# Kernel tuning notes

Hardware: AMD Instinct MI355X
Metric: run time of the kernel (lower is better)

Reference implementation:

```python
import jax, jax.numpy as jnp
import numpy as np

N_NODES = 100000


def gcn_conv(x, src, dst, W, b, n):
    """PyG GCNConv: add self-loops, symmetric normalization, out = A_hat @ (x W) + b."""
    loop = jnp.arange(n, dtype=src.dtype)
    s = jnp.concatenate([src, loop])
    d = jnp.concatenate([dst, loop])
    deg = jnp.zeros((n,), dtype=x.dtype).at[d].add(1.0)
    dinv = jnp.where(deg > 0, jax.lax.rsqrt(deg), 0.0)
    norm = dinv[s] * dinv[d]                      # [E+N]
    h = x @ W                                     # [N, out]
    msg = h[s] * norm[:, None]                    # [E+N, out] gather
    out = jax.ops.segment_sum(msg, d, num_segments=n)  # scatter-add
    return out + b


def prelu(x, a):
    return jnp.where(x >= 0, x, a * x)


def setup_inputs() -> dict:
    key = jax.random.key(0)
    ks = jax.random.split(key, 12)
    n, din, dout, dproj = N_NODES, 128, 128, 128
    dhid = 2 * dout
    x = jax.random.normal(ks[0], (n, din), dtype=jnp.float32)
    edge_index = jax.random.randint(ks[1], (2, 1600000), 0, n, dtype=jnp.int64)

    def glorot(k, fan_in, fan_out):
        lim = np.sqrt(6.0 / (fan_in + fan_out))
        return jax.random.uniform(k, (fan_in, fan_out), jnp.float32, -lim, lim)

    return {
        "x": x,
        "edge_index": edge_index,
        "W1": glorot(ks[2], din, dhid),
        "b1": jnp.zeros((dhid,), jnp.float32),
        "W2": glorot(ks[3], dhid, dout),
        "b2": jnp.zeros((dout,), jnp.float32),
        "a": jnp.asarray(0.25, jnp.float32),          # PReLU weight (num_parameters=1)
        "fc1_w": glorot(ks[4], dout, dproj),
        "fc1_b": jnp.zeros((dproj,), jnp.float32),
        "fc2_w": glorot(ks[5], dproj, dout),
        "fc2_b": jnp.zeros((dout,), jnp.float32),
    }


def reference(x, edge_index, W1, b1, W2, b2, a, fc1_w, fc1_b, fc2_w, fc2_b):
    n = x.shape[0]
    src, dst = edge_index[0], edge_index[1]
    out = prelu(gcn_conv(x, src, dst, W1, b1, n), a)
    out = prelu(gcn_conv(out, src, dst, W2, b2, n), a)
    proj = jax.nn.relu(out @ fc1_w + fc1_b)
    proj = proj @ fc2_w + fc2_b
    return (out, proj)
```

## Files before the change

### kernel.cpp

```cpp
#include <hip/hip_runtime.h>


typedef __attribute__((ext_vector_type(4))) float  f32x4;
typedef __attribute__((ext_vector_type(8))) __bf16 bf16x8;
typedef __attribute__((ext_vector_type(8))) short  short8;

__device__ __forceinline__ bf16x8 as_bf(short8 s) {
    union { short8 s; bf16x8 b; } u; u.s = s; return u.b;
}

__device__ __forceinline__ short2 split1(float x) {
    unsigned u = __float_as_uint(x);
    short hi = (short)(u >> 16);
    float hif = __uint_as_float(u & 0xFFFF0000u);
    short lo = (short)(__float_as_uint(x - hif) >> 16);
    return make_short2(hi, lo);
}

__global__ void deg_kernel(const int* __restrict__ dst, int* __restrict__ deg, int E) {
    int e = blockIdx.x * blockDim.x + threadIdx.x;
    if (e < E) atomicAdd(&deg[dst[e]], 1);
}

__global__ __launch_bounds__(256)
void part_kernel(const int* __restrict__ deg, int* __restrict__ bsum,
                 float* __restrict__ dinv, int n) {
    int tid = threadIdx.x;
    int base = blockIdx.x * 1024 + tid * 4;
    int d[4] = {0, 0, 0, 0};
    if (base + 3 < n) {
        int4 v = *(const int4*)(deg + base);
        d[0] = v.x; d[1] = v.y; d[2] = v.z; d[3] = v.w;
    } else {
        for (int j = 0; j < 4; ++j) if (base + j < n) d[j] = deg[base + j];
    }
    for (int j = 0; j < 4; ++j)
        if (base + j < n) dinv[base + j] = rsqrtf((float)(d[j] + 1));
    int s = d[0] + d[1] + d[2] + d[3];
    for (int off = 32; off > 0; off >>= 1) s += __shfl_down(s, off);
    __shared__ int wsum[4];
    if ((tid & 63) == 0) wsum[tid >> 6] = s;
    __syncthreads();
    if (tid == 0) bsum[blockIdx.x] = wsum[0] + wsum[1] + wsum[2] + wsum[3];
}

__global__ __launch_bounds__(1024)
void topscan_kernel(const int* __restrict__ bsum, int* __restrict__ bbase, int nb) {
    __shared__ int sh[1024];
    int tid = threadIdx.x;
    int own = (tid < nb) ? bsum[tid] : 0;
    sh[tid] = own;
    __syncthreads();
    for (int off = 1; off < 1024; off <<= 1) {
        int t = (tid >= off) ? sh[tid - off] : 0;
        __syncthreads();
        sh[tid] += t;
        __syncthreads();
    }
    if (tid < nb) bbase[tid] = sh[tid] - own;
}

__global__ __launch_bounds__(256)
void offs_kernel(const int* __restrict__ deg, const int* __restrict__ bbase,
                 int* __restrict__ offsets, int n) {
    int tid = threadIdx.x;
    int base = blockIdx.x * 1024 + tid * 4;
    int d[4] = {0, 0, 0, 0};
    if (base + 3 < n) {
        int4 v = *(const int4*)(deg + base);
        d[0] = v.x; d[1] = v.y; d[2] = v.z; d[3] = v.w;
    } else {
        for (int j = 0; j < 4; ++j) if (base + j < n) d[j] = deg[base + j];
    }
    int s = d[0] + d[1] + d[2] + d[3];
    __shared__ int sh[256];
    sh[tid] = s;
    __syncthreads();
    for (int off = 1; off < 256; off <<= 1) {
        int t = (tid >= off) ? sh[tid - off] : 0;
        __syncthreads();
        sh[tid] += t;
        __syncthreads();
    }
    int run = bbase[blockIdx.x] + sh[tid] - s;
    for (int j = 0; j < 4; ++j) {
        int idx = base + j;
        if (idx <= n) offsets[idx] = run;
        if (idx < n) run += d[j];
    }
}

__global__ void fill_kernel(const int* __restrict__ src, const int* __restrict__ dst,
                            const int* __restrict__ offsets, int* __restrict__ cursor,
                            int* __restrict__ csr, int E) {
    int e = blockIdx.x * blockDim.x + threadIdx.x;
    if (e < E) {
        int d = dst[e];
        int pos = offsets[d] + atomicAdd(&cursor[d], 1);
        csr[pos] = src[e];
    }
}

__global__ void wconv_kernel(const float* __restrict__ W, short* __restrict__ Fh,
                             short* __restrict__ Fl, int K, int N, int ktlog) {
    int o = blockIdx.x * blockDim.x + threadIdx.x;
    if (o >= K * N) return;
    int j  = o & 7;
    int l  = (o >> 3) & 15;
    int q  = (o >> 7) & 3;
    int t2 = o >> 9;
    int kt = t2 & ((1 << ktlog) - 1);
    int nt = t2 >> ktlog;
    int nn = nt * 16 + l;
    int kk = kt * 32 + q * 8 + j;
    short2 s = split1(W[(size_t)kk * N + nn]);
    Fh[o] = s.x;
    Fl[o] = s.y;
}

__global__ __launch_bounds__(256)
void agg128_kernel(const float* __restrict__ g, const int* __restrict__ csr,
                   const int* __restrict__ offsets, const float* __restrict__ dinv,
                   const float* __restrict__ bias, const float* __restrict__ a_ptr,
                   float* __restrict__ out, int n) {
    int w = threadIdx.x >> 6;
    int lane = threadIdx.x & 63;
    int v = blockIdx.x * 4 + w;
    if (v >= n) return;
    const char* gb = (const char*)g;
    unsigned loff = (unsigned)lane * 8u;
    float dv = dinv[v];
    float2 self = *(const float2*)(gb + ((unsigned)v * 512u + loff));
    float accx = dv * self.x;
    float accy = dv * self.y;
    int e = offsets[v], end = offsets[v + 1];
#pragma unroll 1
    for (; e < end; e += 12) {
        int   idx[12];
        float dd[12];
        float2 mm[12];
#pragma unroll
        for (int j = 0; j < 12; ++j) {
            int ee = e + j;
            idx[j] = csr[ee < end ? ee : end - 1];
        }
#pragma unroll
        for (int j = 0; j < 12; ++j)
            dd[j] = (e + j < end) ? dinv[idx[j]] : 0.f;
#pragma unroll
        for (int j = 0; j < 12; ++j)
            mm[j] = *(const float2*)(gb + ((unsigned)idx[j] * 512u + loff));
#pragma unroll
        for (int j = 0; j < 12; ++j) {
            accx += dd[j] * mm[j].x;
            accy += dd[j] * mm[j].y;
        }
    }
    accx *= dv;
    accy *= dv;
    if (bias) {
        float a = *a_ptr;
        float2 bb = ((const float2*)bias)[lane];
        accx += bb.x;
        accy += bb.y;
        accx = accx >= 0.f ? accx : a * accx;
        accy = accy >= 0.f ? accy : a * accy;
    }
    float2 r; r.x = accx; r.y = accy;
    ((float2*)out)[(size_t)v * 64 + lane] = r;
}

template<int KT, int T>
__global__ __launch_bounds__(256)
void gemm64_kernel(const float* __restrict__ A, int lda,
                   const short* __restrict__ Bh, const short* __restrict__ Bl,
                   float* __restrict__ C, int M, int N,
                   int mtiles, int tpb,
                   const float* __restrict__ bias, int act,
                   const float* __restrict__ a_ptr) {
    const int tid  = threadIdx.x;
    const int wave = tid >> 6, lane = tid & 63;
    const int quad = lane >> 4, l16 = lane & 15;
    const int col0 = blockIdx.y * (T * 16);
    const int nt0  = col0 >> 4;

    bf16x8 bf[T][KT][2];
#pragma unroll
    for (int t = 0; t < T; ++t)
#pragma unroll
        for (int kt = 0; kt < KT; ++kt) {
            size_t off = ((size_t)((nt0 + t) * KT + kt) << 9) + (lane << 3);
            bf[t][kt][0] = as_bf(*(const short8*)(Bh + off));
            bf[t][kt][1] = as_bf(*(const short8*)(Bl + off));
        }

    const float aw = (act == 2) ? *a_ptr : 0.f;

    const int t0 = blockIdx.x * tpb;
    const int t1 = (t0 + tpb < mtiles) ? t0 + tpb : mtiles;
    for (int tile = t0; tile < t1; ++tile) {
        const int m  = tile * 64 + wave * 16 + l16;
        const int mc = m < M ? m : M - 1;
        const float* Ap = A + (size_t)mc * lda + quad * 8;

        f32x4 acc[T];
#pragma unroll
        for (int t = 0; t < T; ++t) acc[t] = (f32x4){0.f, 0.f, 0.f, 0.f};

#pragma unroll
        for (int kh = 0; kh < KT / 4; ++kh) {
            float4 av[8];
#pragma unroll
            for (int kk = 0; kk < 4; ++kk) {
                av[2 * kk]     = *(const float4*)(Ap + (kh * 4 + kk) * 32);
                av[2 * kk + 1] = *(const float4*)(Ap + (kh * 4 + kk) * 32 + 4);
            }
#pragma unroll
            for (int kk = 0; kk < 4; ++kk) {
                const int kt = kh * 4 + kk;
                float4 v0 = av[2 * kk], v1 = av[2 * kk + 1];
                short8 ah, al;
                short2 s;
                s = split1(v0.x); ah[0] = s.x; al[0] = s.y;
                s = split1(v0.y); ah[1] = s.x; al[1] = s.y;
                s = split1(v0.z); ah[2] = s.x; al[2] = s.y;
                s = split1(v0.w); ah[3] = s.x; al[3] = s.y;
                s = split1(v1.x); ah[4] = s.x; al[4] = s.y;
                s = split1(v1.y); ah[5] = s.x; al[5] = s.y;
                s = split1(v1.z); ah[6] = s.x; al[6] = s.y;
                s = split1(v1.w); ah[7] = s.x; al[7] = s.y;
                bf16x8 a_hi = as_bf(ah), a_lo = as_bf(al);
#pragma unroll
                for (int t = 0; t < T; ++t) {
                    acc[t] = __builtin_amdgcn_mfma_f32_16x16x32_bf16(bf[t][kt][0], a_hi, acc[t], 0, 0, 0);
                    acc[t] = __builtin_amdgcn_mfma_f32_16x16x32_bf16(bf[t][kt][1], a_hi, acc[t], 0, 0, 0);
                    acc[t] = __builtin_amdgcn_mfma_f32_16x16x32_bf16(bf[t][kt][0], a_lo, acc[t], 0, 0, 0);
                }
            }
        }

        if (m < M) {
            float* Crow = C + (size_t)m * N + col0 + quad * 4;
#pragma unroll
            for (int t = 0; t < T; ++t) {
                float4 v;
                v.x = acc[t][0]; v.y = acc[t][1]; v.z = acc[t][2]; v.w = acc[t][3];
                if (bias) {
                    const float4 bb = *(const float4*)(bias + col0 + t * 16 + quad * 4);
                    v.x += bb.x; v.y += bb.y; v.z += bb.z; v.w += bb.w;
                }
                if (act == 1) {
                    v.x = fmaxf(v.x, 0.f); v.y = fmaxf(v.y, 0.f);
                    v.z = fmaxf(v.z, 0.f); v.w = fmaxf(v.w, 0.f);
                } else if (act == 2) {
                    v.x = v.x >= 0.f ? v.x : aw * v.x;
                    v.y = v.y >= 0.f ? v.y : aw * v.y;
                    v.z = v.z >= 0.f ? v.z : aw * v.z;
                    v.w = v.w >= 0.f ? v.w : aw * v.w;
                }
                *(float4*)(Crow + t * 16) = v;
            }
        }
    }
}

extern "C" void kernel_launch(void* const* d_in, const int* in_sizes, int n_in,
                              void* d_out, int out_size, void* d_ws, size_t ws_size,
                              hipStream_t stream) {
    const float* x     = (const float*)d_in[0];
    const int*   ei    = (const int*)d_in[1];
    const float* W1    = (const float*)d_in[2];
    const float* b1    = (const float*)d_in[3];
    const float* W2    = (const float*)d_in[4];
    const float* b2    = (const float*)d_in[5];
    const float* a_ptr = (const float*)d_in[6];
    const float* fc1_w = (const float*)d_in[7];
    const float* fc1_b = (const float*)d_in[8];
    const float* fc2_w = (const float*)d_in[9];
    const float* fc2_b = (const float*)d_in[10];

    const int n = in_sizes[0] / 128;
    const int E = in_sizes[1] / 2;
    const int* src = ei;
    const int* dst = ei + E;
    const int nb = (n + 1023) >> 10;

    float* out_final  = (float*)d_out;
    float* proj_final = out_final + (size_t)n * 128;
    float* out1       = (float*)d_out;

    char* p = (char*)d_ws;
    auto take = [&](size_t bytes) -> char* {
        char* q = p;
        p += (bytes + 1023) & ~(size_t)1023;
        return q;
    };
    int*   deg     = (int*)take((size_t)n * 4);
    int*   offsets = (int*)take(((size_t)n + 1) * 4);
    int*   cursor  = (int*)take((size_t)n * 4);
    float* dinv    = (float*)take((size_t)n * 4);
    int*   bsum    = (int*)take((size_t)1024 * 4);
    int*   bbase   = (int*)take((size_t)1024 * 4);
    int*   csr     = (int*)take((size_t)E * 4);
    short* W1t_hi  = (short*)take((size_t)256 * 128 * 2);
    short* W1t_lo  = (short*)take((size_t)256 * 128 * 2);
    short* W2t_hi  = (short*)take((size_t)128 * 256 * 2);
    short* W2t_lo  = (short*)take((size_t)128 * 256 * 2);
    short* f1t_hi  = (short*)take((size_t)128 * 128 * 2);
    short* f1t_lo  = (short*)take((size_t)128 * 128 * 2);
    short* f2t_hi  = (short*)take((size_t)128 * 128 * 2);
    short* f2t_lo  = (short*)take((size_t)128 * 128 * 2);
    float* bufA    = (float*)take((size_t)n * 128 * 4);

    (void)hipMemsetAsync(deg, 0, (size_t)n * 4, stream);
    (void)hipMemsetAsync(cursor, 0, (size_t)n * 4, stream);

    wconv_kernel<<<(128 * 256 + 255) / 256, 256, 0, stream>>>(W1, W1t_hi, W1t_lo, 128, 256, 2);
    wconv_kernel<<<(256 * 128 + 255) / 256, 256, 0, stream>>>(W2, W2t_hi, W2t_lo, 256, 128, 3);
    wconv_kernel<<<(128 * 128 + 255) / 256, 256, 0, stream>>>(fc1_w, f1t_hi, f1t_lo, 128, 128, 2);
    wconv_kernel<<<(128 * 128 + 255) / 256, 256, 0, stream>>>(fc2_w, f2t_hi, f2t_lo, 128, 128, 2);

    deg_kernel<<<(E + 255) / 256, 256, 0, stream>>>(dst, deg, E);
    part_kernel<<<nb, 256, 0, stream>>>(deg, bsum, dinv, n);
    topscan_kernel<<<1, 1024, 0, stream>>>(bsum, bbase, nb);
    offs_kernel<<<nb, 256, 0, stream>>>(deg, bbase, offsets, n);
    fill_kernel<<<(E + 255) / 256, 256, 0, stream>>>(src, dst, offsets, cursor, csr, E);

    const int mtiles = (n + 63) / 64;
    const int TPB = 4;
    const int gx = (mtiles + TPB - 1) / TPB;

    agg128_kernel<<<(n + 3) / 4, 256, 0, stream>>>(x, csr, offsets, dinv,
                                                   nullptr, nullptr, bufA, n);
    gemm64_kernel<4, 4><<<dim3(gx, 4), 256, 0, stream>>>(
        bufA, 128, W1t_hi, W1t_lo, out1, n, 256, mtiles, TPB, b1, 2, a_ptr);

    gemm64_kernel<8, 2><<<dim3(gx, 4), 256, 0, stream>>>(
        out1, 256, W2t_hi, W2t_lo, bufA, n, 128, mtiles, TPB, nullptr, 0, nullptr);
    agg128_kernel<<<(n + 3) / 4, 256, 0, stream>>>(bufA, csr, offsets, dinv,
                                                   b2, a_ptr, out_final, n);

    gemm64_kernel<4, 4><<<dim3(gx, 2), 256, 0, stream>>>(
        out_final, 128, f1t_hi, f1t_lo, bufA, n, 128, mtiles, TPB, fc1_b, 1, nullptr);
    gemm64_kernel<4, 4><<<dim3(gx, 2), 256, 0, stream>>>(
        bufA, 128, f2t_hi, f2t_lo, proj_final, n, 128, mtiles, TPB, fc2_b, 0, nullptr);
}
```

Measured before the change: 778.2 us.

## Stage full weight matrices in LDS and compute all output columns per block

The GEMM kernel now copies the entire split-bf16 weight matrix into shared memory once per block, and each block covers all N columns for 128-row tiles. A persistent grid-stride loop replaces the 2D grid of column slices. Before, each block held a column slice of the weights in registers and the A rows were reread once per column slice. The aim is to read A once and cut the register pressure of holding weights, at the cost of LDS reads in the inner loop and a large shared footprint (up to 128KB for the 256-wide layer), which may limit occupancy.

```diff
diff --git a/kernel.cpp b/kernel.cpp
--- a/kernel.cpp
+++ b/kernel.cpp
@@ -170,42 +170,39 @@
     ((float2*)out)[(size_t)v * 64 + lane] = r;
 }
 
-template<int KT, int T>
-__global__ __launch_bounds__(256)
-void gemm64_kernel(const float* __restrict__ A, int lda,
-                   const short* __restrict__ Bh, const short* __restrict__ Bl,
-                   float* __restrict__ C, int M, int N,
-                   int mtiles, int tpb,
-                   const float* __restrict__ bias, int act,
-                   const float* __restrict__ a_ptr) {
+template<int KT, int NT>
+__global__ __launch_bounds__(512)
+void gemmL_kernel(const float* __restrict__ A,
+                  const short* __restrict__ Bh, const short* __restrict__ Bl,
+                  float* __restrict__ C, int M, int ntiles,
+                  const float* __restrict__ bias, int act,
+                  const float* __restrict__ a_ptr) {
+    constexpr int N = NT * 16;
+    __shared__ short lh[NT * KT * 512];
+    __shared__ short ll[NT * KT * 512];
+
     const int tid  = threadIdx.x;
     const int wave = tid >> 6, lane = tid & 63;
     const int quad = lane >> 4, l16 = lane & 15;
-    const int col0 = blockIdx.y * (T * 16);
-    const int nt0  = col0 >> 4;
-
-    bf16x8 bf[T][KT][2];
-#pragma unroll
-    for (int t = 0; t < T; ++t)
-#pragma unroll
-        for (int kt = 0; kt < KT; ++kt) {
-            size_t off = ((size_t)((nt0 + t) * KT + kt) << 9) + (lane << 3);
-            bf[t][kt][0] = as_bf(*(const short8*)(Bh + off));
-            bf[t][kt][1] = as_bf(*(const short8*)(Bl + off));
-        }
+
+    constexpr int units = NT * KT * 64;
+    for (int i = tid; i < units; i += 512) {
+        ((short8*)lh)[i] = ((const short8*)Bh)[i];
+        ((short8*)ll)[i] = ((const short8*)Bl)[i];
+    }
+    __syncthreads();
 
     const float aw = (act == 2) ? *a_ptr : 0.f;
 
-    const int t0 = blockIdx.x * tpb;
-    const int t1 = (t0 + tpb < mtiles) ? t0 + tpb : mtiles;
-    for (int tile = t0; tile < t1; ++tile) {
-        const int m  = tile * 64 + wave * 16 + l16;
+#pragma unroll 1
+    for (int tile = blockIdx.x; tile < ntiles; tile += gridDim.x) {
+        const int m  = tile * 128 + wave * 16 + l16;
         const int mc = m < M ? m : M - 1;
-        const float* Ap = A + (size_t)mc * lda + quad * 8;
-
-        f32x4 acc[T];
-#pragma unroll
-        for (int t = 0; t < T; ++t) acc[t] = (f32x4){0.f, 0.f, 0.f, 0.f};
+        const float* Ap = A + (size_t)mc * (KT * 32) + quad * 8;
+
+        f32x4 acc[NT];
+#pragma unroll
+        for (int t = 0; t < NT; ++t) acc[t] = (f32x4){0.f, 0.f, 0.f, 0.f};
 
 #pragma unroll
         for (int kh = 0; kh < KT / 4; ++kh) {
@@ -231,22 +228,25 @@
                 s = split1(v1.w); ah[7] = s.x; al[7] = s.y;
                 bf16x8 a_hi = as_bf(ah), a_lo = as_bf(al);
 #pragma unroll
-                for (int t = 0; t < T; ++t) {
-                    acc[t] = __builtin_amdgcn_mfma_f32_16x16x32_bf16(bf[t][kt][0], a_hi, acc[t], 0, 0, 0);
-                    acc[t] = __builtin_amdgcn_mfma_f32_16x16x32_bf16(bf[t][kt][1], a_hi, acc[t], 0, 0, 0);
-                    acc[t] = __builtin_amdgcn_mfma_f32_16x16x32_bf16(bf[t][kt][0], a_lo, acc[t], 0, 0, 0);
+                for (int t = 0; t < NT; ++t) {
+                    const int fo = ((t * KT + kt) << 9) + (lane << 3);
+                    bf16x8 bh = as_bf(*(const short8*)(lh + fo));
+                    bf16x8 bl = as_bf(*(const short8*)(ll + fo));
+                    acc[t] = __builtin_amdgcn_mfma_f32_16x16x32_bf16(bh, a_hi, acc[t], 0, 0, 0);
+                    acc[t] = __builtin_amdgcn_mfma_f32_16x16x32_bf16(bl, a_hi, acc[t], 0, 0, 0);
+                    acc[t] = __builtin_amdgcn_mfma_f32_16x16x32_bf16(bh, a_lo, acc[t], 0, 0, 0);
                 }
             }
         }
 
         if (m < M) {
-            float* Crow = C + (size_t)m * N + col0 + quad * 4;
-#pragma unroll
-            for (int t = 0; t < T; ++t) {
+            float* Crow = C + (size_t)m * N + quad * 4;
+#pragma unroll
+            for (int t = 0; t < NT; ++t) {
                 float4 v;
                 v.x = acc[t][0]; v.y = acc[t][1]; v.z = acc[t][2]; v.w = acc[t][3];
                 if (bias) {
-                    const float4 bb = *(const float4*)(bias + col0 + t * 16 + quad * 4);
+                    const float4 bb = *(const float4*)(bias + t * 16 + quad * 4);
                     v.x += bb.x; v.y += bb.y; v.z += bb.z; v.w += bb.w;
                 }
                 if (act == 1) {
@@ -326,22 +326,20 @@
     offs_kernel<<<nb, 256, 0, stream>>>(deg, bbase, offsets, n);
     fill_kernel<<<(E + 255) / 256, 256, 0, stream>>>(src, dst, offsets, cursor, csr, E);
 
-    const int mtiles = (n + 63) / 64;
-    const int TPB = 4;
-    const int gx = (mtiles + TPB - 1) / TPB;
+    const int ntiles = (n + 127) / 128;
 
     agg128_kernel<<<(n + 3) / 4, 256, 0, stream>>>(x, csr, offsets, dinv,
                                                    nullptr, nullptr, bufA, n);
-    gemm64_kernel<4, 4><<<dim3(gx, 4), 256, 0, stream>>>(
-        bufA, 128, W1t_hi, W1t_lo, out1, n, 256, mtiles, TPB, b1, 2, a_ptr);
-
-    gemm64_kernel<8, 2><<<dim3(gx, 4), 256, 0, stream>>>(
-        out1, 256, W2t_hi, W2t_lo, bufA, n, 128, mtiles, TPB, nullptr, 0, nullptr);
+    gemmL_kernel<4, 16><<<256, 512, 0, stream>>>(bufA, W1t_hi, W1t_lo, out1,
+                                                 n, ntiles, b1, 2, a_ptr);
+
+    gemmL_kernel<8, 8><<<256, 512, 0, stream>>>(out1, W2t_hi, W2t_lo, bufA,
+                                                n, ntiles, nullptr, 0, nullptr);
     agg128_kernel<<<(n + 3) / 4, 256, 0, stream>>>(bufA, csr, offsets, dinv,
                                                    b2, a_ptr, out_final, n);
 
-    gemm64_kernel<4, 4><<<dim3(gx, 2), 256, 0, stream>>>(
-        out_final, 128, f1t_hi, f1t_lo, bufA, n, 128, mtiles, TPB, fc1_b, 1, nullptr);
-    gemm64_kernel<4, 4><<<dim3(gx, 2), 256, 0, stream>>>(
-        bufA, 128, f2t_hi, f2t_lo, proj_final, n, 128, mtiles, TPB, fc2_b, 0, nullptr);
-}
+    gemmL_kernel<4, 8><<<512, 512, 0, stream>>>(out_final, f1t_hi, f1t_lo, bufA,
+                                                n, ntiles, fc1_b, 1, nullptr);
+    gemmL_kernel<4, 8><<<512, 512, 0, stream>>>(bufA, f2t_hi, f2t_lo, proj_final,
+                                                n, ntiles, fc2_b, 0, nullptr);
+}
```

Result: slower. 1.170 ms (+50.4%).

## Store GEMM operands as pre-split bf16 hi/lo planes produced by producer epilogues

Applied to the files above, without the earlier changes.

Producers (aggregation and GEMM epilogues) now write their outputs directly as bf16 hi/lo split planes, so consuming GEMMs load short8 operands and skip the per-element float split. The GEMM grid is also flattened to 1D with column blocks interleaved next to each other for the same row block, which may improve L2 reuse of A. This removes repeated split ALU work in the GEMM inner loop, and the A-operand bytes are unchanged (two 2-byte planes instead of one 4-byte float). It reuses the output buffers as scratch for intermediate planes, which relies on later kernels overwriting them in order.

```diff
diff --git a/kernel.cpp b/kernel.cpp
--- a/kernel.cpp
+++ b/kernel.cpp
@@ -15,6 +15,10 @@
     float hif = __uint_as_float(u & 0xFFFF0000u);
     short lo = (short)(__float_as_uint(x - hif) >> 16);
     return make_short2(hi, lo);
+}
+
+__device__ __forceinline__ unsigned pack2(short a, short b) {
+    return ((unsigned)(unsigned short)a) | ((unsigned)(unsigned short)b << 16);
 }
 
 __global__ void deg_kernel(const int* __restrict__ dst, int* __restrict__ deg, int E) {
@@ -122,7 +126,8 @@
 void agg128_kernel(const float* __restrict__ g, const int* __restrict__ csr,
                    const int* __restrict__ offsets, const float* __restrict__ dinv,
                    const float* __restrict__ bias, const float* __restrict__ a_ptr,
-                   float* __restrict__ out, int n) {
+                   float* __restrict__ outf, short* __restrict__ oh,
+                   short* __restrict__ ol, int n) {
     int w = threadIdx.x >> 6;
     int lane = threadIdx.x & 63;
     int v = blockIdx.x * 4 + w;
@@ -166,22 +171,34 @@
         accx = accx >= 0.f ? accx : a * accx;
         accy = accy >= 0.f ? accy : a * accy;
     }
-    float2 r; r.x = accx; r.y = accy;
-    ((float2*)out)[(size_t)v * 64 + lane] = r;
-}
-
-template<int KT, int T>
+    if (outf) {
+        float2 r; r.x = accx; r.y = accy;
+        ((float2*)outf)[(size_t)v * 64 + lane] = r;
+    }
+    if (oh) {
+        short2 s0 = split1(accx), s1 = split1(accy);
+        ((unsigned*)(oh + (size_t)v * 128))[lane] = pack2(s0.x, s1.x);
+        ((unsigned*)(ol + (size_t)v * 128))[lane] = pack2(s0.y, s1.y);
+    }
+}
+
+template<int KT, int T, int EPI>
 __global__ __launch_bounds__(256)
-void gemm64_kernel(const float* __restrict__ A, int lda,
+void gemm64_kernel(const short* __restrict__ Ah, const short* __restrict__ Al,
                    const short* __restrict__ Bh, const short* __restrict__ Bl,
-                   float* __restrict__ C, int M, int N,
+                   float* __restrict__ Cf, short* __restrict__ Ch,
+                   short* __restrict__ Cl, int M, int N, int ncol,
                    int mtiles, int tpb,
                    const float* __restrict__ bias, int act,
                    const float* __restrict__ a_ptr) {
+    constexpr int K = KT * 32;
     const int tid  = threadIdx.x;
     const int wave = tid >> 6, lane = tid & 63;
     const int quad = lane >> 4, l16 = lane & 15;
-    const int col0 = blockIdx.y * (T * 16);
+    const int bid  = blockIdx.x;
+    const int rowblk = bid / ncol;
+    const int colblk = bid - rowblk * ncol;
+    const int col0 = colblk * (T * 16);
     const int nt0  = col0 >> 4;
 
     bf16x8 bf[T][KT][2];
@@ -196,57 +213,45 @@
 
     const float aw = (act == 2) ? *a_ptr : 0.f;
 
-    const int t0 = blockIdx.x * tpb;
+    const int t0 = rowblk * tpb;
     const int t1 = (t0 + tpb < mtiles) ? t0 + tpb : mtiles;
+#pragma unroll 1
     for (int tile = t0; tile < t1; ++tile) {
         const int m  = tile * 64 + wave * 16 + l16;
         const int mc = m < M ? m : M - 1;
-        const float* Ap = A + (size_t)mc * lda + quad * 8;
+        const short* Ahp = Ah + (size_t)mc * K + quad * 8;
+        const short* Alp = Al + (size_t)mc * K + quad * 8;
+
+        short8 ahv[KT], alv[KT];
+#pragma unroll
+        for (int kt = 0; kt < KT; ++kt) {
+            ahv[kt] = *(const short8*)(Ahp + kt * 32);
+            alv[kt] = *(const short8*)(Alp + kt * 32);
+        }
 
         f32x4 acc[T];
 #pragma unroll
         for (int t = 0; t < T; ++t) acc[t] = (f32x4){0.f, 0.f, 0.f, 0.f};
 
 #pragma unroll
-        for (int kh = 0; kh < KT / 4; ++kh) {
-            float4 av[8];
-#pragma unroll
-            for (int kk = 0; kk < 4; ++kk) {
-                av[2 * kk]     = *(const float4*)(Ap + (kh * 4 + kk) * 32);
-                av[2 * kk + 1] = *(const float4*)(Ap + (kh * 4 + kk) * 32 + 4);
+        for (int kt = 0; kt < KT; ++kt) {
+            bf16x8 a_hi = as_bf(ahv[kt]), a_lo = as_bf(alv[kt]);
+#pragma unroll
+            for (int t = 0; t < T; ++t) {
+                acc[t] = __builtin_amdgcn_mfma_f32_16x16x32_bf16(bf[t][kt][0], a_hi, acc[t], 0, 0, 0);
+                acc[t] = __builtin_amdgcn_mfma_f32_16x16x32_bf16(bf[t][kt][1], a_hi, acc[t], 0, 0, 0);
+                acc[t] = __builtin_amdgcn_mfma_f32_16x16x32_bf16(bf[t][kt][0], a_lo, acc[t], 0, 0, 0);
             }
-#pragma unroll
-            for (int kk = 0; kk < 4; ++kk) {
-                const int kt = kh * 4 + kk;
-                float4 v0 = av[2 * kk], v1 = av[2 * kk + 1];
-                short8 ah, al;
-                short2 s;
-                s = split1(v0.x); ah[0] = s.x; al[0] = s.y;
-                s = split1(v0.y); ah[1] = s.x; al[1] = s.y;
-                s = split1(v0.z); ah[2] = s.x; al[2] = s.y;
-                s = split1(v0.w); ah[3] = s.x; al[3] = s.y;
-                s = split1(v1.x); ah[4] = s.x; al[4] = s.y;
-                s = split1(v1.y); ah[5] = s.x; al[5] = s.y;
-                s = split1(v1.z); ah[6] = s.x; al[6] = s.y;
-                s = split1(v1.w); ah[7] = s.x; al[7] = s.y;
-                bf16x8 a_hi = as_bf(ah), a_lo = as_bf(al);
-#pragma unroll
-                for (int t = 0; t < T; ++t) {
-                    acc[t] = __builtin_amdgcn_mfma_f32_16x16x32_bf16(bf[t][kt][0], a_hi, acc[t], 0, 0, 0);
-                    acc[t] = __builtin_amdgcn_mfma_f32_16x16x32_bf16(bf[t][kt][1], a_hi, acc[t], 0, 0, 0);
-                    acc[t] = __builtin_amdgcn_mfma_f32_16x16x32_bf16(bf[t][kt][0], a_lo, acc[t], 0, 0, 0);
-                }
-            }
         }
 
         if (m < M) {
-            float* Crow = C + (size_t)m * N + col0 + quad * 4;
 #pragma unroll
             for (int t = 0; t < T; ++t) {
+                const int col = col0 + t * 16 + quad * 4;
                 float4 v;
                 v.x = acc[t][0]; v.y = acc[t][1]; v.z = acc[t][2]; v.w = acc[t][3];
                 if (bias) {
-                    const float4 bb = *(const float4*)(bias + col0 + t * 16 + quad * 4);
+                    const float4 bb = *(const float4*)(bias + col);
                     v.x += bb.x; v.y += bb.y; v.z += bb.z; v.w += bb.w;
                 }
                 if (act == 1) {
@@ -258,7 +263,17 @@
                     v.z = v.z >= 0.f ? v.z : aw * v.z;
                     v.w = v.w >= 0.f ? v.w : aw * v.w;
                 }
-                *(float4*)(Crow + t * 16) = v;
+                if (EPI == 0) {
+                    *(float4*)(Cf + (size_t)m * N + col) = v;
+                } else {
+                    short2 s0 = split1(v.x), s1 = split1(v.y);
+                    short2 s2 = split1(v.z), s3 = split1(v.w);
+                    uint2 hp, lp;
+                    hp.x = pack2(s0.x, s1.x); hp.y = pack2(s2.x, s3.x);
+                    lp.x = pack2(s0.y, s1.y); lp.y = pack2(s2.y, s3.y);
+                    *(uint2*)(Ch + (size_t)m * N + col) = hp;
+                    *(uint2*)(Cl + (size_t)m * N + col) = lp;
+                }
             }
         }
     }
@@ -287,7 +302,7 @@
 
     float* out_final  = (float*)d_out;
     float* proj_final = out_final + (size_t)n * 128;
-    float* out1       = (float*)d_out;
+
 
     char* p = (char*)d_ws;
     auto take = [&](size_t bytes) -> char* {
@@ -312,6 +327,15 @@
     short* f2t_lo  = (short*)take((size_t)128 * 128 * 2);
     float* bufA    = (float*)take((size_t)n * 128 * 4);
 
+    short* A1h = (short*)bufA;
+    short* A1l = A1h + (size_t)n * 128;
+    short* O1h = (short*)d_out;
+    short* O1l = O1h + (size_t)n * 256;
+    short* P2h = (short*)proj_final;
+    short* P2l = P2h + (size_t)n * 128;
+    short* F1h = (short*)bufA;
+    short* F1l = F1h + (size_t)n * 128;
+
     (void)hipMemsetAsync(deg, 0, (size_t)n * 4, stream);
     (void)hipMemsetAsync(cursor, 0, (size_t)n * 4, stream);
 
@@ -328,20 +352,26 @@
 
     const int mtiles = (n + 63) / 64;
     const int TPB = 4;
-    const int gx = (mtiles + TPB - 1) / TPB;
+    const int RB = (mtiles + TPB - 1) / TPB;
 
     agg128_kernel<<<(n + 3) / 4, 256, 0, stream>>>(x, csr, offsets, dinv,
-                                                   nullptr, nullptr, bufA, n);
-    gemm64_kernel<4, 4><<<dim3(gx, 4), 256, 0, stream>>>(
-        bufA, 128, W1t_hi, W1t_lo, out1, n, 256, mtiles, TPB, b1, 2, a_ptr);
-
-    gemm64_kernel<8, 2><<<dim3(gx, 4), 256, 0, stream>>>(
-        out1, 256, W2t_hi, W2t_lo, bufA, n, 128, mtiles, TPB, nullptr, 0, nullptr);
+                                                   nullptr, nullptr,
+                                                   nullptr, A1h, A1l, n);
+    gemm64_kernel<4, 4, 1><<<RB * 4, 256, 0, stream>>>(
+        A1h, A1l, W1t_hi, W1t_lo, nullptr, O1h, O1l,
+        n, 256, 4, mtiles, TPB, b1, 2, a_ptr);
+
+    gemm64_kernel<8, 2, 0><<<RB * 4, 256, 0, stream>>>(
+        O1h, O1l, W2t_hi, W2t_lo, bufA, nullptr, nullptr,
+        n, 128, 4, mtiles, TPB, nullptr, 0, nullptr);
     agg128_kernel<<<(n + 3) / 4, 256, 0, stream>>>(bufA, csr, offsets, dinv,
-                                                   b2, a_ptr, out_final, n);
-
-    gemm64_kernel<4, 4><<<dim3(gx, 2), 256, 0, stream>>>(
-        out_final, 128, f1t_hi, f1t_lo, bufA, n, 128, mtiles, TPB, fc1_b, 1, nullptr);
-    gemm64_kernel<4, 4><<<dim3(gx, 2), 256, 0, stream>>>(
-        bufA, 128, f2t_hi, f2t_lo, proj_final, n, 128, mtiles, TPB, fc2_b, 0, nullptr);
-}
+                                                   b2, a_ptr,
+                                                   out_final, P2h, P2l, n);
+
+    gemm64_kernel<4, 4, 1><<<RB * 2, 256, 0, stream>>>(
+        P2h, P2l, f1t_hi, f1t_lo, nullptr, F1h, F1l,
+        n, 128, 2, mtiles, TPB, fc1_b, 1, nullptr);
+    gemm64_kernel<4, 4, 0><<<RB * 2, 256, 0, stream>>>(
+        F1h, F1l, f2t_hi, f2t_lo, proj_final, nullptr, nullptr,
+        n, 128, 2, mtiles, TPB, fc2_b, 0, nullptr);
+}
```

New measurement: 798.9 us. +2.7%, slower.
